# Performance work log

Hardware: AMD Instinct MI355X
Metric: run time of the kernel (lower is better)

The kernel has to match this reference:

```python
import jax, jax.numpy as jnp
import numpy as np

N_NODES = 100000
N_EDGES = 3200000
N_FEAT = 512
H_MLP = 256
H_GCN = 256
N_CLS = 40


def setup_inputs() -> dict:
    key = jax.random.key(0)
    ks = jax.random.split(key, 8)
    s = 0.02
    return {
        "x": jax.random.normal(ks[0], (N_NODES, N_FEAT), jnp.float32),
        "edge_index": jax.random.randint(ks[1], (2, N_EDGES), 0, N_NODES, dtype=jnp.int64),
        "W_mlp": jax.random.normal(ks[2], (N_FEAT, H_MLP), jnp.float32) * s,
        "b_mlp": jnp.zeros((H_MLP,), jnp.float32),
        "W1": jax.random.normal(ks[3], (H_MLP, H_GCN), jnp.float32) * s,
        "b1": jnp.zeros((H_GCN,), jnp.float32),
        "W2": jax.random.normal(ks[4], (H_GCN, N_CLS), jnp.float32) * s,
        "b2": jnp.zeros((N_CLS,), jnp.float32),
    }


def _gcn_aggregate(h, row, col, edge_norm, self_coef, n):
    # h: [N, D]; messages along edges col->row with symmetric normalization,
    # plus the self-loop term deg^-1 * h (GCNConv default add_self_loops=True).
    msgs = h[col] * edge_norm[:, None]              # [E, D]
    agg = jax.ops.segment_sum(msgs, row, num_segments=n)
    return agg + h * self_coef[:, None]


def reference(x, edge_index, W_mlp, b_mlp, W1, b1, W2, b2):
    n = x.shape[0]
    row, col = edge_index[0], edge_index[1]
    # degree with self-loops (PyG gcn_norm counts edge weight into col, +1 self-loop)
    deg = jax.ops.segment_sum(jnp.ones(row.shape[0], x.dtype), col, num_segments=n) + 1.0
    dis = jax.lax.rsqrt(deg)                         # deg^-1/2, [N]
    edge_norm = dis[row] * dis[col]                  # [E]
    self_coef = dis * dis                            # deg^-1 for self loops, [N]

    h = jax.nn.relu(x @ W_mlp + b_mlp)               # [N, H_MLP]
    h = _gcn_aggregate(h @ W1, row, col, edge_norm, self_coef, n) + b1
    h = jax.nn.relu(h)
    # dropout is identity in eval mode (F.dropout with training=False)
    out = _gcn_aggregate(h @ W2, row, col, edge_norm, self_coef, n) + b2
    return out
```

## Files before the change

### kernel.cpp

```cpp
#include <hip/hip_runtime.h>

#define NN 100000
#define NE 3200000
#define NF 512
#define NH 256
#define NC 40

#define CH 32768
#define NCH 4
#define NPAD (NCH * CH)
#define PARTS 64
#define SLICE ((NE + PARTS - 1) / PARTS)
#define NBLK ((NN + 255) / 256)

typedef __attribute__((ext_vector_type(8))) short bf16x8;
typedef __attribute__((ext_vector_type(4))) float f32x4;
typedef __attribute__((ext_vector_type(4))) unsigned short u16x4;
typedef __attribute__((ext_vector_type(8))) unsigned short u16x8;

__device__ inline unsigned short f2bf(float f) {
    union { float f; unsigned u; } v; v.f = f;
    unsigned r = v.u + 0x7fffu + ((v.u >> 16) & 1u);
    return (unsigned short)(r >> 16);
}
__device__ inline float bf2f(unsigned short s) {
    union { unsigned u; float f; } v; v.u = ((unsigned)s) << 16;
    return v.f;
}


__global__ __launch_bounds__(512) void hist2_kernel(const int* __restrict__ ei,
                                                    unsigned char* __restrict__ rpart8,
                                                    unsigned char* __restrict__ cpart8) {
    __shared__ unsigned h[CH / 2];
    const int chunk = blockIdx.x, part = blockIdx.y, which = blockIdx.z;
    const int* src = which ? (ei + NE) : ei;
    unsigned char* outp = which ? cpart8 : rpart8;
    const int lo = chunk * CH;
    for (int i = threadIdx.x; i < CH / 2; i += 512) h[i] = 0;
    __syncthreads();
    const int e1 = min((part + 1) * SLICE, NE);
    for (int e = part * SLICE + threadIdx.x; e < e1; e += 512) {
        unsigned v = (unsigned)(src[e] - lo);
        if (v < CH) atomicAdd(&h[v >> 1], 1u << ((v & 1) << 4));
    }
    __syncthreads();
    unsigned char* dst = outp + (size_t)part * NPAD + lo;
    for (int i = threadIdx.x; i < CH; i += 512)
        dst[i] = (unsigned char)((h[i >> 1] >> ((i & 1) << 4)) & 0xffu);
}

__global__ __launch_bounds__(256) void reduce_kernel(const unsigned char* __restrict__ rpart8,
                                                     const unsigned char* __restrict__ cpart8,
                                                     int* __restrict__ row_cnt, float* __restrict__ dis,
                                                     int* __restrict__ bsum) {
    __shared__ int s[256];
    const int tid = threadIdx.x;
    const int v = blockIdx.x * 256 + tid;
    unsigned rs = 0, cs = 0;
    if (v < NN) {
        #pragma unroll 1
        for (int p = 0; p < PARTS; p++) {
            rs += rpart8[(size_t)p * NPAD + v];
            cs += cpart8[(size_t)p * NPAD + v];
        }
        row_cnt[v] = (int)rs;
        dis[v] = rsqrtf((float)cs + 1.0f);
    }
    s[tid] = (int)rs;
    __syncthreads();
    #pragma unroll
    for (int o = 128; o > 0; o >>= 1) {
        if (tid < o) s[tid] += s[tid + o];
        __syncthreads();
    }
    if (tid == 0) bsum[blockIdx.x] = s[0];
}

__global__ __launch_bounds__(512) void scanb_kernel(const int* __restrict__ bsum,
                                                    int* __restrict__ boff) {
    __shared__ int s[512];
    const int t = threadIdx.x;
    int v = (t < NBLK) ? bsum[t] : 0;
    s[t] = v;
    __syncthreads();
    #pragma unroll
    for (int o = 1; o < 512; o <<= 1) {
        int u = (t >= o) ? s[t - o] : 0;
        __syncthreads();
        s[t] += u;
        __syncthreads();
    }
    if (t < NBLK) boff[t] = s[t] - v;
}

__global__ __launch_bounds__(256) void rstart2_kernel(const unsigned char* __restrict__ rpart8,
                                                      const int* __restrict__ row_cnt,
                                                      const int* __restrict__ boff,
                                                      int* __restrict__ row_ptr,
                                                      unsigned* __restrict__ rbase) {
    __shared__ int s[256];
    const int tid = threadIdx.x;
    const int v = blockIdx.x * 256 + tid;
    int cnt = (v < NN) ? row_cnt[v] : 0;
    s[tid] = cnt;
    __syncthreads();
    #pragma unroll
    for (int o = 1; o < 256; o <<= 1) {
        int u = (tid >= o) ? s[tid - o] : 0;
        __syncthreads();
        s[tid] += u;
        __syncthreads();
    }
    if (v < NN) {
        unsigned run = (unsigned)(boff[blockIdx.x] + s[tid] - cnt);
        row_ptr[v] = (int)run;
        #pragma unroll 1
        for (int p = 0; p < PARTS; p++) {
            size_t i = (size_t)p * NPAD + v;
            rbase[i] = run;
            run += rpart8[i];
        }
    }
    if (v == NN) row_ptr[NN] = NE;
}

__global__ __launch_bounds__(512) void fill2d_kernel(const int* __restrict__ ei,
                                                     const unsigned* __restrict__ rbase,
                                                     int* __restrict__ csr) {
    __shared__ unsigned cur[CH / 2];
    const int bid = blockIdx.x;
    const int xcd = bid & 7;
    const int chunk = xcd >> 1;
    const int part = ((bid >> 3) << 1) | (xcd & 1);
    const int lo = chunk * CH;
    for (int i = threadIdx.x; i < CH / 2; i += 512) cur[i] = 0;
    __syncthreads();
    const unsigned* base = rbase + (size_t)part * NPAD + lo;
    const int e1 = min((part + 1) * SLICE, NE);
    for (int e = part * SLICE + threadIdx.x; e < e1; e += 512) {
        int r = ei[e];
        unsigned rr = (unsigned)(r - lo);
        if (rr < CH) {
            int c = ei[NE + e];
            unsigned sh = (rr & 1) << 4;
            unsigned old = atomicAdd(&cur[rr >> 1], 1u << sh);
            unsigned p = (old >> sh) & 0xffffu;
            csr[base[rr] + p] = c;
        }
    }
}

__global__ void wtrans_all(const float* __restrict__ Wm, const float* __restrict__ W1,
                           const float* __restrict__ W2, unsigned short* __restrict__ WTm,
                           unsigned short* __restrict__ W1T, unsigned short* __restrict__ W2T) {
    int t = blockIdx.x * 256 + threadIdx.x;
    if (t < NH * NF) {
        int n = t / NF, k = t % NF;
        int sw = ((k >> 3) & 3) ^ (n & 3) ^ ((n >> 2) & 3);
        WTm[n * NF + (k & ~31) + (sw << 3) + (k & 7)] = f2bf(Wm[(long)k * NH + n]);
        return;
    }
    t -= NH * NF;
    if (t < NH * NH) {
        int n = t / NH, k = t % NH;
        int sw = ((k >> 3) & 3) ^ (n & 3) ^ ((n >> 2) & 3);
        W1T[n * NH + (k & ~31) + (sw << 3) + (k & 7)] = f2bf(W1[(long)k * NH + n]);
        return;
    }
    t -= NH * NH;
    if (t < 64 * NH) {
        int n = t / NH, k = t % NH;
        int sw = ((k >> 3) & 3) ^ (n & 3) ^ ((n >> 2) & 3);
        W2T[n * NH + (k & ~31) + (sw << 3) + (k & 7)] =
            (n < NC) ? f2bf(W2[(long)k * NC + n]) : (unsigned short)0;
    }
}

__global__ __launch_bounds__(512)
void gemm12_kernel(const float* __restrict__ x, const unsigned short* __restrict__ WTm,
                   const float* __restrict__ bmlp, const unsigned short* __restrict__ W1T,
                   unsigned short* __restrict__ t1, int M) {
    __shared__ short h0s[128 * 256];
    __shared__ short Bs2[256 * 32];

    const int tid = threadIdx.x;
    const int lane = tid & 63;
    const int wid = tid >> 6;
    const int wr = wid >> 1;
    const int wc = wid & 1;
    const long bm = (long)blockIdx.x * 128;
    const int l15 = lane & 15, g = lane >> 4, l4 = lane >> 4;

    f32x4 acc[2][8];
    #pragma unroll
    for (int i = 0; i < 2; i++)
        #pragma unroll
        for (int j = 0; j < 8; j++) acc[i][j] = (f32x4){0.f, 0.f, 0.f, 0.f};

    for (int k0 = 0; k0 < NF; k0 += 32) {
        #pragma unroll
        for (int i = 0; i < 2; i++) {
            int ch = tid + i * 512;
            __builtin_amdgcn_global_load_lds(
                (const void*)(WTm + (size_t)(ch >> 2) * NF + k0 + (ch & 3) * 8),
                (void*)(&h0s[4096 + ch * 8]), 16, 0, 0);
        }
        {
            int ch = tid;
            int row = ch >> 2, c = ch & 3;
            int sw = c ^ (row & 3) ^ ((row >> 2) & 3);
            long gr = bm + row;
            bf16x8 w = (bf16x8){0, 0, 0, 0, 0, 0, 0, 0};
            if (gr < M) {
                float4 v0 = *(const float4*)(x + gr * NF + k0 + c * 8);
                float4 v1 = *(const float4*)(x + gr * NF + k0 + c * 8 + 4);
                w[0] = (short)f2bf(v0.x); w[1] = (short)f2bf(v0.y);
                w[2] = (short)f2bf(v0.z); w[3] = (short)f2bf(v0.w);
                w[4] = (short)f2bf(v1.x); w[5] = (short)f2bf(v1.y);
                w[6] = (short)f2bf(v1.z); w[7] = (short)f2bf(v1.w);
            }
            *(bf16x8*)(&h0s[row * 32 + sw * 8]) = w;
        }
        __syncthreads();

        bf16x8 a[2];
        #pragma unroll
        for (int mi = 0; mi < 2; mi++) {
            int row = wr * 32 + mi * 16 + l15;
            int sw = g ^ (row & 3) ^ ((row >> 2) & 3);
            a[mi] = *(const bf16x8*)(&h0s[row * 32 + sw * 8]);
        }
        #pragma unroll
        for (int ni = 0; ni < 8; ni++) {
            int row = wc * 128 + ni * 16 + l15;
            int sw = g ^ (row & 3) ^ ((row >> 2) & 3);
            bf16x8 b = *(const bf16x8*)(&h0s[4096 + row * 32 + sw * 8]);
            #pragma unroll
            for (int mi = 0; mi < 2; mi++)
                acc[mi][ni] = __builtin_amdgcn_mfma_f32_16x16x32_bf16(a[mi], b, acc[mi][ni], 0, 0, 0);
        }
        __syncthreads();
    }

    #pragma unroll
    for (int mi = 0; mi < 2; mi++) {
        int r0 = wr * 32 + mi * 16 + l4 * 4;
        #pragma unroll
        for (int ni = 0; ni < 8; ni++) {
            int gc = wc * 128 + ni * 16 + l15;
            float bv = bmlp[gc];
            int cc = gc >> 3, c7 = gc & 7;
            #pragma unroll
            for (int q = 0; q < 4; q++) {
                int row = r0 + q;
                float v = fmaxf(acc[mi][ni][q] + bv, 0.f);
                h0s[row * 256 + ((cc ^ (row & 7)) << 3) + c7] = (short)f2bf(v);
            }
        }
    }

    #pragma unroll
    for (int i = 0; i < 2; i++)
        #pragma unroll
        for (int j = 0; j < 8; j++) acc[i][j] = (f32x4){0.f, 0.f, 0.f, 0.f};

    for (int k2 = 0; k2 < NH; k2 += 32) {
        #pragma unroll
        for (int i = 0; i < 2; i++) {
            int ch = tid + i * 512;
            __builtin_amdgcn_global_load_lds(
                (const void*)(W1T + (size_t)(ch >> 2) * NH + k2 + (ch & 3) * 8),
                (void*)(&Bs2[ch * 8]), 16, 0, 0);
        }
        __syncthreads();

        bf16x8 a[2];
        #pragma unroll
        for (int mi = 0; mi < 2; mi++) {
            int row = wr * 32 + mi * 16 + l15;
            int cc = (k2 >> 3) + g;
            a[mi] = *(const bf16x8*)(&h0s[row * 256 + ((cc ^ (row & 7)) << 3)]);
        }
        #pragma unroll
        for (int ni = 0; ni < 8; ni++) {
            int row = wc * 128 + ni * 16 + l15;
            int sw = g ^ (row & 3) ^ ((row >> 2) & 3);
            bf16x8 b = *(const bf16x8*)(&Bs2[row * 32 + sw * 8]);
            #pragma unroll
            for (int mi = 0; mi < 2; mi++)
                acc[mi][ni] = __builtin_amdgcn_mfma_f32_16x16x32_bf16(a[mi], b, acc[mi][ni], 0, 0, 0);
        }
        __syncthreads();
    }

    #pragma unroll
    for (int mi = 0; mi < 2; mi++) {
        long gr0 = bm + wr * 32 + mi * 16 + l4 * 4;
        #pragma unroll
        for (int ni = 0; ni < 8; ni++) {
            int gc = wc * 128 + ni * 16 + l15;
            #pragma unroll
            for (int q = 0; q < 4; q++) {
                long gr = gr0 + q;
                if (gr < M) t1[gr * NH + gc] = f2bf(acc[mi][ni][q]);
            }
        }
    }
}

__global__ __launch_bounds__(256)
void gemm3_kernel(const unsigned short* __restrict__ A, const unsigned short* __restrict__ W2T,
                  unsigned short* __restrict__ C, int M) {
    constexpr int BM = 128, BK = 32;
    __shared__ short As[BM * BK];
    __shared__ short Bs[64 * BK];

    const int tid = threadIdx.x;
    const int lane = tid & 63;
    const int wid = tid >> 6;
    const int wr = wid;
    const long bm = (long)blockIdx.x * BM;
    const int l15 = lane & 15, g = lane >> 4, l4 = lane >> 4;

    f32x4 acc[2][4];
    #pragma unroll
    for (int i = 0; i < 2; i++)
        #pragma unroll
        for (int j = 0; j < 4; j++) acc[i][j] = (f32x4){0.f, 0.f, 0.f, 0.f};

    for (int k0 = 0; k0 < NH; k0 += BK) {
        {
            int ch = tid;
            __builtin_amdgcn_global_load_lds(
                (const void*)(W2T + (size_t)(ch >> 2) * NH + k0 + (ch & 3) * 8),
                (void*)(&Bs[ch * 8]), 16, 0, 0);
        }
        #pragma unroll
        for (int i = 0; i < 2; i++) {
            int ch = tid + i * 256;
            int row = ch >> 2, c = ch & 3;
            int sw = c ^ (row & 3) ^ ((row >> 2) & 3);
            long gr = bm + row;
            bf16x8 w = (bf16x8){0, 0, 0, 0, 0, 0, 0, 0};
            if (gr < M) w = *(const bf16x8*)(A + gr * NH + k0 + c * 8);
            *(bf16x8*)(&As[row * BK + sw * 8]) = w;
        }
        __syncthreads();

        bf16x8 a[2];
        #pragma unroll
        for (int mi = 0; mi < 2; mi++) {
            int row = wr * 32 + mi * 16 + l15;
            int sw = g ^ (row & 3) ^ ((row >> 2) & 3);
            a[mi] = *(const bf16x8*)(&As[row * BK + sw * 8]);
        }
        #pragma unroll
        for (int ni = 0; ni < 4; ni++) {
            int row = ni * 16 + l15;
            int sw = g ^ (row & 3) ^ ((row >> 2) & 3);
            bf16x8 b = *(const bf16x8*)(&Bs[row * BK + sw * 8]);
            #pragma unroll
            for (int mi = 0; mi < 2; mi++)
                acc[mi][ni] = __builtin_amdgcn_mfma_f32_16x16x32_bf16(a[mi], b, acc[mi][ni], 0, 0, 0);
        }
        __syncthreads();
    }

    #pragma unroll
    for (int mi = 0; mi < 2; mi++) {
        long gr0 = bm + wr * 32 + mi * 16 + l4 * 4;
        #pragma unroll
        for (int ni = 0; ni < 4; ni++) {
            int gc = ni * 16 + l15;
            if (gc >= NC) continue;
            #pragma unroll
            for (int q = 0; q < 4; q++) {
                long gr = gr0 + q;
                if (gr < M) C[gr * NC + gc] = f2bf(acc[mi][ni][q]);
            }
        }
    }
}

__global__ void agg256_kernel(const unsigned short* __restrict__ t, const int* __restrict__ row_ptr,
                              const int* __restrict__ csr, const float* __restrict__ dis,
                              const float* __restrict__ bias, unsigned short* __restrict__ out, int n) {
    const int wid = threadIdx.x >> 6, lane = threadIdx.x & 63;
    const int node = blockIdx.x * 4 + wid;
    if (node >= n) return;
    const int half = lane >> 5;
    const int f0 = (lane & 31) * 8;
    const float d = dis[node];
    float a[8];
    if (half == 0) {
        u16x8 sv = *(const u16x8*)(t + (long)node * NH + f0);
        float d2 = d * d;
        #pragma unroll
        for (int j = 0; j < 8; j++) a[j] = bf2f(sv[j]) * d2;
    } else {
        #pragma unroll
        for (int j = 0; j < 8; j++) a[j] = 0.f;
    }
    const int lo = row_ptr[node], hi = row_ptr[node + 1];
    int ee = lo + half;
    for (; ee + 6 < hi; ee += 8) {
        int c0 = csr[ee], c1 = csr[ee + 2], c2 = csr[ee + 4], c3 = csr[ee + 6];
        float w0 = d * dis[c0], w1 = d * dis[c1];
        float w2 = d * dis[c2], w3 = d * dis[c3];
        u16x8 v0 = *(const u16x8*)(t + (long)c0 * NH + f0);
        u16x8 v1 = *(const u16x8*)(t + (long)c1 * NH + f0);
        u16x8 v2 = *(const u16x8*)(t + (long)c2 * NH + f0);
        u16x8 v3 = *(const u16x8*)(t + (long)c3 * NH + f0);
        #pragma unroll
        for (int j = 0; j < 8; j++)
            a[j] += (bf2f(v0[j]) * w0 + bf2f(v1[j]) * w1) + (bf2f(v2[j]) * w2 + bf2f(v3[j]) * w3);
    }
    for (; ee + 2 < hi; ee += 4) {
        int c0 = csr[ee], c1 = csr[ee + 2];
        float w0 = d * dis[c0], w1 = d * dis[c1];
        u16x8 v0 = *(const u16x8*)(t + (long)c0 * NH + f0);
        u16x8 v1 = *(const u16x8*)(t + (long)c1 * NH + f0);
        #pragma unroll
        for (int j = 0; j < 8; j++)
            a[j] += bf2f(v0[j]) * w0 + bf2f(v1[j]) * w1;
    }
    if (ee < hi) {
        int c0 = csr[ee];
        float w0 = d * dis[c0];
        u16x8 v0 = *(const u16x8*)(t + (long)c0 * NH + f0);
        #pragma unroll
        for (int j = 0; j < 8; j++) a[j] += bf2f(v0[j]) * w0;
    }
    #pragma unroll
    for (int j = 0; j < 8; j++) a[j] += __shfl_xor(a[j], 32);
    if (half == 0) {
        u16x8 o;
        #pragma unroll
        for (int j = 0; j < 8; j++)
            o[j] = f2bf(fmaxf(a[j] + bias[f0 + j], 0.f));
        *(u16x8*)(out + (long)node * NH + f0) = o;
    }
}

__global__ void agg40_kernel(const unsigned short* __restrict__ t, const int* __restrict__ row_ptr,
                             const int* __restrict__ csr, const float* __restrict__ dis,
                             const float* __restrict__ bias, float* __restrict__ out, int n) {
    const int wid = threadIdx.x >> 6, lane = threadIdx.x & 63;
    const int node = blockIdx.x * 4 + wid;
    if (node >= n) return;
    const int g = lane >> 3;
    const int f0 = (lane & 7) * 8;
    const bool act = f0 < NC;
    const float d = dis[node];
    float a[8];
    #pragma unroll
    for (int j = 0; j < 8; j++) a[j] = 0.f;
    const int lo = row_ptr[node], hi = row_ptr[node + 1];
    if (act) {
        if (g == 0) {
            u16x8 sv = *(const u16x8*)(t + (long)node * NC + f0);
            float d2 = d * d;
            #pragma unroll
            for (int j = 0; j < 8; j++) a[j] = bf2f(sv[j]) * d2;
        }
        int ee = lo + g;
        for (; ee + 8 < hi; ee += 16) {
            int c0 = csr[ee], c1 = csr[ee + 8];
            float w0 = d * dis[c0], w1 = d * dis[c1];
            u16x8 v0 = *(const u16x8*)(t + (long)c0 * NC + f0);
            u16x8 v1 = *(const u16x8*)(t + (long)c1 * NC + f0);
            #pragma unroll
            for (int j = 0; j < 8; j++)
                a[j] += bf2f(v0[j]) * w0 + bf2f(v1[j]) * w1;
        }
        if (ee < hi) {
            int c0 = csr[ee];
            float w0 = d * dis[c0];
            u16x8 v0 = *(const u16x8*)(t + (long)c0 * NC + f0);
            #pragma unroll
            for (int j = 0; j < 8; j++) a[j] += bf2f(v0[j]) * w0;
        }
    }
    #pragma unroll
    for (int s = 8; s < 64; s <<= 1)
        #pragma unroll
        for (int j = 0; j < 8; j++) a[j] += __shfl_xor(a[j], s);
    if (g == 0 && act) {
        float4 o0, o1;
        o0.x = a[0] + bias[f0 + 0]; o0.y = a[1] + bias[f0 + 1];
        o0.z = a[2] + bias[f0 + 2]; o0.w = a[3] + bias[f0 + 3];
        o1.x = a[4] + bias[f0 + 4]; o1.y = a[5] + bias[f0 + 5];
        o1.z = a[6] + bias[f0 + 6]; o1.w = a[7] + bias[f0 + 7];
        float* dst = out + (long)node * NC + f0;
        *(float4*)dst = o0;
        *(float4*)(dst + 4) = o1;
    }
}


extern "C" void kernel_launch(void* const* d_in, const int* in_sizes, int n_in,
                              void* d_out, int out_size, void* d_ws, size_t ws_size,
                              hipStream_t stream) {
    const float* x     = (const float*)d_in[0];
    const int*   ei    = (const int*)d_in[1];
    const float* W_mlp = (const float*)d_in[2];
    const float* b_mlp = (const float*)d_in[3];
    const float* W1    = (const float*)d_in[4];
    const float* b1    = (const float*)d_in[5];
    const float* W2    = (const float*)d_in[6];
    const float* b2    = (const float*)d_in[7];
    float* out = (float*)d_out;

    float* ws = (float*)d_ws;
    size_t off = 0;
    float*    dis     = ws + off; off += 100096;
    int*      row_cnt = (int*)(ws + off); off += 100096;
    int*      row_ptr = (int*)(ws + off); off += 100096;
    int*      bsum    = (int*)(ws + off); off += 512;
    int*      boff    = (int*)(ws + off); off += 512;
    unsigned char* rpart8 = (unsigned char*)(ws + off); off += (size_t)PARTS * NPAD / 4;
    unsigned char* cpart8 = (unsigned char*)(ws + off); off += (size_t)PARTS * NPAD / 4;
    unsigned* rbase   = (unsigned*)(ws + off); off += (size_t)PARTS * NPAD;
    int*      csr     = (int*)(ws + off); off += (size_t)NE;
    unsigned short* WTm = (unsigned short*)(ws + off); off += (NH * NF) / 2;
    unsigned short* W1T = (unsigned short*)(ws + off); off += (NH * NH) / 2;
    unsigned short* W2T = (unsigned short*)(ws + off); off += (64 * NH) / 2;
    unsigned short* t1  = (unsigned short*)(ws + off); off += (size_t)NN * NH / 2;
    unsigned short* h1  = (unsigned short*)(ws + off); off += (size_t)NN * NH / 2;
    unsigned short* t2p = (unsigned short*)(ws + off); off += ((size_t)NN * NC + 8) / 2;
    (void)ws_size;

    dim3 gh(NCH, PARTS, 2);
    hist2_kernel<<<gh, 512, 0, stream>>>(ei, rpart8, cpart8);
    reduce_kernel<<<NBLK, 256, 0, stream>>>(rpart8, cpart8, row_cnt, dis, bsum);
    scanb_kernel<<<1, 512, 0, stream>>>(bsum, boff);
    rstart2_kernel<<<NBLK, 256, 0, stream>>>(rpart8, row_cnt, boff, row_ptr, rbase);
    fill2d_kernel<<<NCH * PARTS, 512, 0, stream>>>(ei, rbase, csr);

    wtrans_all<<<(NH * NF + NH * NH + 64 * NH + 255) / 256, 256, 0, stream>>>(
        W_mlp, W1, W2, WTm, W1T, W2T);

    const int mb = (NN + 127) / 128;
    gemm12_kernel<<<mb, 512, 0, stream>>>(x, WTm, b_mlp, W1T, t1, NN);
    agg256_kernel<<<(NN + 3) / 4, 256, 0, stream>>>(t1, row_ptr, csr, dis, b1, h1, NN);
    gemm3_kernel<<<mb, 256, 0, stream>>>(h1, W2T, t2p, NN);
    agg40_kernel<<<(NN + 3) / 4, 256, 0, stream>>>(t2p, row_ptr, csr, dis, b2, out, NN);
}
```

Before: 600.1 us.

## Store hidden features in 16-column planes and aggregate plane-by-plane with LDS edge cache

The first hidden layer's output t1 and h1 are now stored as 16 feature planes of 16 columns each, so each plane is 3.2 MB and has a better chance of staying cache-resident during the random gather. The new aggregation kernel handles 128 nodes per block. It caches their column indices and edge weights in LDS, then loops over the 16 planes so the same edges are reused per plane. It also undoes the XCD-aware block mapping in fill2d, going back to a plain 2D grid. The cost is 16 passes over the edge lists, 8-byte gathers in place of 16-byte ones, and possible load imbalance inside a block.

```diff
diff --git a/kernel.cpp b/kernel.cpp
--- a/kernel.cpp
+++ b/kernel.cpp
@@ -12,6 +12,11 @@
 #define PARTS 64
 #define SLICE ((NE + PARTS - 1) / PARTS)
 #define NBLK ((NN + 255) / 256)
+
+#define GB 16
+#define GF 16
+#define NPB 128
+#define ECAP 8192
 
 typedef __attribute__((ext_vector_type(8))) short bf16x8;
 typedef __attribute__((ext_vector_type(4))) float f32x4;
@@ -129,10 +134,7 @@
                                                      const unsigned* __restrict__ rbase,
                                                      int* __restrict__ csr) {
     __shared__ unsigned cur[CH / 2];
-    const int bid = blockIdx.x;
-    const int xcd = bid & 7;
-    const int chunk = xcd >> 1;
-    const int part = ((bid >> 3) << 1) | (xcd & 1);
+    const int chunk = blockIdx.x, part = blockIdx.y;
     const int lo = chunk * CH;
     for (int i = threadIdx.x; i < CH / 2; i += 512) cur[i] = 0;
     __syncthreads();
@@ -300,10 +302,11 @@
         #pragma unroll
         for (int ni = 0; ni < 8; ni++) {
             int gc = wc * 128 + ni * 16 + l15;
+            unsigned short* pl = t1 + (size_t)(gc >> 4) * NN * GF + (gc & 15);
             #pragma unroll
             for (int q = 0; q < 4; q++) {
                 long gr = gr0 + q;
-                if (gr < M) t1[gr * NH + gc] = f2bf(acc[mi][ni][q]);
+                if (gr < M) pl[gr * GF] = f2bf(acc[mi][ni][q]);
             }
         }
     }
@@ -342,8 +345,9 @@
             int row = ch >> 2, c = ch & 3;
             int sw = c ^ (row & 3) ^ ((row >> 2) & 3);
             long gr = bm + row;
+            int k = k0 + c * 8;
             bf16x8 w = (bf16x8){0, 0, 0, 0, 0, 0, 0, 0};
-            if (gr < M) w = *(const bf16x8*)(A + gr * NH + k0 + c * 8);
+            if (gr < M) w = *(const bf16x8*)(A + (size_t)(k >> 4) * NN * GF + gr * GF + (k & 15));
             *(bf16x8*)(&As[row * BK + sw * 8]) = w;
         }
         __syncthreads();
@@ -383,63 +387,82 @@
     }
 }
 
-__global__ void agg256_kernel(const unsigned short* __restrict__ t, const int* __restrict__ row_ptr,
-                              const int* __restrict__ csr, const float* __restrict__ dis,
-                              const float* __restrict__ bias, unsigned short* __restrict__ out, int n) {
-    const int wid = threadIdx.x >> 6, lane = threadIdx.x & 63;
-    const int node = blockIdx.x * 4 + wid;
-    if (node >= n) return;
-    const int half = lane >> 5;
-    const int f0 = (lane & 31) * 8;
-    const float d = dis[node];
-    float a[8];
-    if (half == 0) {
-        u16x8 sv = *(const u16x8*)(t + (long)node * NH + f0);
-        float d2 = d * d;
-        #pragma unroll
-        for (int j = 0; j < 8; j++) a[j] = bf2f(sv[j]) * d2;
-    } else {
-        #pragma unroll
-        for (int j = 0; j < 8; j++) a[j] = 0.f;
-    }
-    const int lo = row_ptr[node], hi = row_ptr[node + 1];
-    int ee = lo + half;
-    for (; ee + 6 < hi; ee += 8) {
-        int c0 = csr[ee], c1 = csr[ee + 2], c2 = csr[ee + 4], c3 = csr[ee + 6];
-        float w0 = d * dis[c0], w1 = d * dis[c1];
-        float w2 = d * dis[c2], w3 = d * dis[c3];
-        u16x8 v0 = *(const u16x8*)(t + (long)c0 * NH + f0);
-        u16x8 v1 = *(const u16x8*)(t + (long)c1 * NH + f0);
-        u16x8 v2 = *(const u16x8*)(t + (long)c2 * NH + f0);
-        u16x8 v3 = *(const u16x8*)(t + (long)c3 * NH + f0);
-        #pragma unroll
-        for (int j = 0; j < 8; j++)
-            a[j] += (bf2f(v0[j]) * w0 + bf2f(v1[j]) * w1) + (bf2f(v2[j]) * w2 + bf2f(v3[j]) * w3);
-    }
-    for (; ee + 2 < hi; ee += 4) {
-        int c0 = csr[ee], c1 = csr[ee + 2];
-        float w0 = d * dis[c0], w1 = d * dis[c1];
-        u16x8 v0 = *(const u16x8*)(t + (long)c0 * NH + f0);
-        u16x8 v1 = *(const u16x8*)(t + (long)c1 * NH + f0);
-        #pragma unroll
-        for (int j = 0; j < 8; j++)
-            a[j] += bf2f(v0[j]) * w0 + bf2f(v1[j]) * w1;
-    }
-    if (ee < hi) {
-        int c0 = csr[ee];
-        float w0 = d * dis[c0];
-        u16x8 v0 = *(const u16x8*)(t + (long)c0 * NH + f0);
-        #pragma unroll
-        for (int j = 0; j < 8; j++) a[j] += bf2f(v0[j]) * w0;
-    }
-    #pragma unroll
-    for (int j = 0; j < 8; j++) a[j] += __shfl_xor(a[j], 32);
-    if (half == 0) {
-        u16x8 o;
-        #pragma unroll
-        for (int j = 0; j < 8; j++)
-            o[j] = f2bf(fmaxf(a[j] + bias[f0 + j], 0.f));
-        *(u16x8*)(out + (long)node * NH + f0) = o;
+__global__ __launch_bounds__(512)
+void aggB_kernel(const unsigned short* __restrict__ tg, const int* __restrict__ row_ptr,
+                 const int* __restrict__ csr, const float* __restrict__ dis,
+                 const float* __restrict__ bias, unsigned short* __restrict__ outg, int n) {
+    __shared__ int colsL[ECAP];
+    __shared__ float wL[ECAP];
+    __shared__ int rp[NPB + 1];
+
+    const int tid = threadIdx.x;
+    const int node0 = blockIdx.x * NPB;
+    for (int i = tid; i <= NPB; i += 512) rp[i] = row_ptr[min(node0 + i, n)];
+    __syncthreads();
+    const int base = rp[0];
+
+    const int cl = tid >> 2;
+    const int fl4 = (tid & 3) * 4;
+    const int node = node0 + cl;
+    const bool valid = node < n;
+    int lo = rp[cl], hi = rp[cl + 1];
+    float d = valid ? dis[node] : 0.f;
+
+    for (int e = lo + (tid & 3); e < hi; e += 4) {
+        int idx = e - base;
+        if (idx < ECAP) {
+            int c = csr[e];
+            colsL[idx] = c;
+            wL[idx] = d * dis[c];
+        }
+    }
+    __syncthreads();
+
+    const float d2 = d * d;
+    #pragma unroll 1
+    for (int g = 0; g < GB; g++) {
+        const unsigned short* pl = tg + (size_t)g * NN * GF;
+        if (valid) {
+            u16x4 sv = *(const u16x4*)(pl + (size_t)node * GF + fl4);
+            float a0 = bf2f(sv[0]) * d2, a1 = bf2f(sv[1]) * d2;
+            float a2 = bf2f(sv[2]) * d2, a3 = bf2f(sv[3]) * d2;
+            int e = lo;
+            for (; e + 1 < hi; e += 2) {
+                int i0 = e - base;
+                int c0, c1; float w0, w1;
+                if (i0 + 1 < ECAP) {
+                    c0 = colsL[i0]; w0 = wL[i0];
+                    c1 = colsL[i0 + 1]; w1 = wL[i0 + 1];
+                } else {
+                    c0 = csr[e]; w0 = d * dis[c0];
+                    c1 = csr[e + 1]; w1 = d * dis[c1];
+                }
+                u16x4 v0 = *(const u16x4*)(pl + (size_t)c0 * GF + fl4);
+                u16x4 v1 = *(const u16x4*)(pl + (size_t)c1 * GF + fl4);
+                a0 += bf2f(v0[0]) * w0 + bf2f(v1[0]) * w1;
+                a1 += bf2f(v0[1]) * w0 + bf2f(v1[1]) * w1;
+                a2 += bf2f(v0[2]) * w0 + bf2f(v1[2]) * w1;
+                a3 += bf2f(v0[3]) * w0 + bf2f(v1[3]) * w1;
+            }
+            if (e < hi) {
+                int i0 = e - base;
+                int c0; float w0;
+                if (i0 < ECAP) { c0 = colsL[i0]; w0 = wL[i0]; }
+                else { c0 = csr[e]; w0 = d * dis[c0]; }
+                u16x4 v0 = *(const u16x4*)(pl + (size_t)c0 * GF + fl4);
+                a0 += bf2f(v0[0]) * w0; a1 += bf2f(v0[1]) * w0;
+                a2 += bf2f(v0[2]) * w0; a3 += bf2f(v0[3]) * w0;
+            }
+            const int f0 = g * GF + fl4;
+            u16x4 o;
+            o[0] = f2bf(fmaxf(a0 + bias[f0 + 0], 0.f));
+            o[1] = f2bf(fmaxf(a1 + bias[f0 + 1], 0.f));
+            o[2] = f2bf(fmaxf(a2 + bias[f0 + 2], 0.f));
+            o[3] = f2bf(fmaxf(a3 + bias[f0 + 3], 0.f));
+            union { u16x4 v; unsigned long long u; } cv; cv.v = o;
+            __builtin_nontemporal_store(cv.u,
+                (unsigned long long*)(outg + (size_t)g * NN * GF + (size_t)node * GF + fl4));
+        }
     }
 }
 
@@ -536,14 +559,15 @@
     reduce_kernel<<<NBLK, 256, 0, stream>>>(rpart8, cpart8, row_cnt, dis, bsum);
     scanb_kernel<<<1, 512, 0, stream>>>(bsum, boff);
     rstart2_kernel<<<NBLK, 256, 0, stream>>>(rpart8, row_cnt, boff, row_ptr, rbase);
-    fill2d_kernel<<<NCH * PARTS, 512, 0, stream>>>(ei, rbase, csr);
+    dim3 gf(NCH, PARTS);
+    fill2d_kernel<<<gf, 512, 0, stream>>>(ei, rbase, csr);
 
     wtrans_all<<<(NH * NF + NH * NH + 64 * NH + 255) / 256, 256, 0, stream>>>(
         W_mlp, W1, W2, WTm, W1T, W2T);
 
     const int mb = (NN + 127) / 128;
     gemm12_kernel<<<mb, 512, 0, stream>>>(x, WTm, b_mlp, W1T, t1, NN);
-    agg256_kernel<<<(NN + 3) / 4, 256, 0, stream>>>(t1, row_ptr, csr, dis, b1, h1, NN);
+    aggB_kernel<<<(NN + NPB - 1) / NPB, 512, 0, stream>>>(t1, row_ptr, csr, dis, b1, h1, NN);
     gemm3_kernel<<<mb, 256, 0, stream>>>(h1, W2T, t2p, NN);
     agg40_kernel<<<(NN + 3) / 4, 256, 0, stream>>>(t2p, row_ptr, csr, dis, b2, out, NN);
 }
```

Result: slower. 892.7 us (+48.8%).
